# Optimization experiments

Hardware: AMD Instinct MI355X
Metric: run time of the kernel (lower is better)

Reference implementation:

```python
import jax, jax.numpy as jnp
import numpy as np
import math

H = 8
E = 512
D_K = E // H
NEG = -1000000000.0
# last (and only surviving) row of dist_bar: one threshold per head
DIST_BAR = np.array([0.2, 0.3, 0.4, 0.5, 0.6, 0.7, 0.8, 0.9], dtype=np.float32)


def setup_inputs() -> dict:
    key = jax.random.key(0)
    ks = jax.random.split(key, 12)
    B, N = 8, 1024
    s = 1.0 / math.sqrt(E)
    inp = {
        "query": jax.random.normal(ks[0], (B, N, E), jnp.float32),
        "key": jax.random.normal(ks[1], (B, N, E), jnp.float32),
        "value": jax.random.normal(ks[2], (B, N, E), jnp.float32),
        "dist": jax.random.uniform(ks[3], (B, 1, N, N), jnp.float32),
        "mask": jnp.ones((B, N, N), jnp.int32),
        "Wq": jax.random.normal(ks[4], (E, E), jnp.float32) * s,
        "bq": jnp.zeros((E,), jnp.float32),
        "Wk": jax.random.normal(ks[5], (E, E), jnp.float32) * s,
        "bk": jnp.zeros((E,), jnp.float32),
        "Wv": jax.random.normal(ks[6], (E, E), jnp.float32) * s,
        "bv": jnp.zeros((E,), jnp.float32),
        "Wo": jax.random.normal(ks[7], (E, E), jnp.float32) * s,
        "bo": jnp.zeros((E,), jnp.float32),
    }
    return inp


def reference(query, key, value, dist, mask, Wq, bq, Wk, bk, Wv, bv, Wo, bo):
    B, N, _ = query.shape
    # project and split heads: [B, H, N, D_K]
    def heads(x, W, b):
        return (x @ W.T + b).reshape(B, N, H, D_K).transpose(0, 2, 1, 3)
    q = heads(query, Wq, bq)
    k = heads(key, Wk, bk)
    v = heads(value, Wv, bv)
    scores = jnp.einsum("bhqd,bhkd->bhqk", q, k) / math.sqrt(D_K)
    # padding mask: [B,N,N] -> [B,1,N,N]
    scores = jnp.where(mask[:, None, :, :] == 0, NEG, scores)
    # per-head distance mask: dist [B,1,N,N] < thr[h] -> [B,H,N,N]
    thr = jnp.asarray(DIST_BAR)[None, :, None, None]
    dmask = dist < thr
    # first row/col (global atom) always attend
    dmask = dmask.at[:, :, 0, :].set(True).at[:, :, :, 0].set(True)
    scores = jnp.where(dmask, scores, NEG)
    p = jax.nn.softmax(scores, axis=-1)
    out = jnp.einsum("bhqk,bhkd->bhqd", p, v)  # [B,H,N,D_K]
    out = out.transpose(0, 2, 1, 3).reshape(B, N, H * D_K)
    return out @ Wo.T + bo
```

## Files before the change

kernel.cpp:

```cpp
#include <hip/hip_runtime.h>
#include <stdint.h>


typedef __attribute__((ext_vector_type(8))) short short8;
typedef __attribute__((ext_vector_type(4))) float floatx4;

#define MFMA16(a, b, c) __builtin_amdgcn_mfma_f32_16x16x32_bf16((a), (b), (c), 0, 0, 0)
#define QSCALE 0.1803368801111362f

static __device__ __forceinline__ unsigned short f2bf(float f) {
  union { float f; unsigned u; } v; v.f = f;
  unsigned r = v.u + 0x7fffu + ((v.u >> 16) & 1u);
  return (unsigned short)(r >> 16);
}

static __device__ __forceinline__ void gload_lds16(const void* g, void* l) {
  __builtin_amdgcn_global_load_lds((const __attribute__((address_space(1))) unsigned int*)g,
                                   (__attribute__((address_space(3))) unsigned int*)l,
                                   16, 0, 0);
}
static __device__ __forceinline__ int xsw(int row) { return (row & 3) ^ ((row >> 2) & 3); }

__global__ void prep_kernel(const float* __restrict__ q, const float* __restrict__ k,
                            const float* __restrict__ v,
                            const float* __restrict__ wq, const float* __restrict__ wk,
                            const float* __restrict__ wv, const float* __restrict__ wo,
                            const float* __restrict__ dist, const int* __restrict__ mask,
                            unsigned short* __restrict__ qb, unsigned short* __restrict__ kb,
                            unsigned short* __restrict__ vb,
                            unsigned short* __restrict__ wq16, unsigned short* __restrict__ wk16,
                            unsigned short* __restrict__ wv16, unsigned short* __restrict__ wo16,
                            unsigned char* __restrict__ codesP) {
  int gb = blockIdx.x;
  if (gb < 13312) {
    int i = gb * 256 + threadIdx.x;
    const float* s; unsigned short* d; int loc;
    if (i < 3145728) {
      int w = i >> 20; loc = i & 1048575;
      s = (w == 0) ? q : (w == 1) ? k : v;
      d = (w == 0) ? qb : (w == 1) ? kb : vb;
    } else {
      int j = i - 3145728; int w = j >> 16; loc = j & 65535;
      s = (w == 0) ? wq : (w == 1) ? wk : (w == 2) ? wv : wo;
      d = (w == 0) ? wq16 : (w == 1) ? wk16 : (w == 2) ? wv16 : wo16;
    }
    float4 vv = ((const float4*)s)[loc];
    ushort4 o;
    o.x = f2bf(vv.x); o.y = f2bf(vv.y); o.z = f2bf(vv.z); o.w = f2bf(vv.w);
    ((ushort4*)d)[loc] = o;
  } else {
    int t = (gb - 13312) * 256 + threadIdx.x;
    int flat = t << 2;
    int b = flat >> 20;
    int rem = flat & ((1 << 20) - 1);
    int row = rem >> 10;
    int col0 = rem & 1023;
    float4 d4 = ((const float4*)dist)[t];
    int4 m4 = ((const int4*)mask)[t];
    float dv[4] = {d4.x, d4.y, d4.z, d4.w};
    int mv[4] = {m4.x, m4.y, m4.z, m4.w};
    int rg = row >> 5;
    int st = (row >> 4) & 1;
    int qq = (row >> 2) & 3;
    int r = row & 3;
    size_t rowbase = (size_t)(b * 32 + rg) * 32768;
    int sub = st * 32 + r;
#pragma unroll
    for (int u = 0; u < 4; u++) {
      int col = col0 + u;
      float d = dv[u];
      int hmin = (d >= 0.2f) + (d >= 0.3f) + (d >= 0.4f) + (d >= 0.5f) +
                 (d >= 0.6f) + (d >= 0.7f) + (d >= 0.8f) + (d >= 0.9f);
      unsigned char cc = (unsigned char)hmin;
      if (row == 0 || col == 0) cc = 0;
      if (mv[u] == 0) cc = 9;
      int kt = col >> 7, ci = (col >> 4) & 7, c = col & 15;
      int lane = qq * 16 + c;
      codesP[rowbase + (size_t)kt * 4096 + lane * 64 + sub + ci * 4] = cc;
    }
  }
}

__global__ __launch_bounds__(256) void qkv_gemm(
    const unsigned short* __restrict__ Xq, const unsigned short* __restrict__ Xk,
    const unsigned short* __restrict__ Xv,
    const unsigned short* __restrict__ Wqp, const unsigned short* __restrict__ Wkp,
    const unsigned short* __restrict__ Wvp,
    const float* __restrict__ bq, const float* __restrict__ bk, const float* __restrict__ bv,
    unsigned short* __restrict__ Qh, unsigned short* __restrict__ Kh,
    unsigned short* __restrict__ Vt) {
  const int z = blockIdx.z;
  const unsigned short* X = (z == 0) ? Xq : (z == 1) ? Xk : Xv;
  const unsigned short* W = (z == 0) ? Wqp : (z == 1) ? Wkp : Wvp;
  const float* bias = (z == 0) ? bq : (z == 1) ? bk : bv;
  unsigned short* O = (z == 0) ? Qh : (z == 1) ? Kh : Vt;

  __shared__ __align__(16) short Xs[128 * 32];
  __shared__ __align__(16) short Ws[128 * 32];
  const int tid = threadIdx.x;
  const int lane = tid & 63;
  const int wave = tid >> 6;
  const int c = lane & 15;
  const int q = lane >> 4;
  const int m0 = blockIdx.x * 128;
  const int n0 = blockIdx.y * 128;
  const int wr = (wave >> 1) * 64;
  const int wc = (wave & 1) * 64;

  floatx4 acc[4][4];
#pragma unroll
  for (int i = 0; i < 4; i++)
#pragma unroll
    for (int j = 0; j < 4; j++) acc[i][j] = (floatx4)(0.0f);

  for (int k0 = 0; k0 < 512; k0 += 32) {
    __syncthreads();
#pragma unroll
    for (int it = 0; it < 2; it++) {
      int slot = wave * 128 + it * 64 + lane;
      int row = slot >> 2, ch = slot & 3;
      int g = ch ^ xsw(row);
      gload_lds16(X + (size_t)(m0 + row) * 512 + k0 + g * 8, &Xs[(wave * 128 + it * 64) * 8]);
      gload_lds16(W + (size_t)(n0 + row) * 512 + k0 + g * 8, &Ws[(wave * 128 + it * 64) * 8]);
    }
    __syncthreads();

    const short* Pa = (z == 2) ? Xs : Ws;
    const short* Pb = (z == 2) ? Ws : Xs;
    short8 af[4], bfv[4];
#pragma unroll
    for (int i = 0; i < 4; i++) {
      int row = wr + i * 16 + c;
      af[i] = *(const short8*)(&Pa[row * 32 + (q ^ xsw(row)) * 8]);
    }
#pragma unroll
    for (int j = 0; j < 4; j++) {
      int row = wc + j * 16 + c;
      bfv[j] = *(const short8*)(&Pb[row * 32 + (q ^ xsw(row)) * 8]);
    }
#pragma unroll
    for (int i = 0; i < 4; i++)
#pragma unroll
      for (int j = 0; j < 4; j++)
        acc[i][j] = MFMA16(af[i], bfv[j], acc[i][j]);
  }

  if (z == 2) {
#pragma unroll
    for (int i = 0; i < 4; i++) {
      int gm0 = m0 + wr + i * 16 + q * 4;
      int b = gm0 >> 10, n = gm0 & 1023;
#pragma unroll
      for (int j = 0; j < 4; j++) {
        int gn = n0 + wc + j * 16 + c;
        float bb = bias[gn];
        int h = gn >> 6, d = gn & 63;
        ushort4 pk;
#pragma unroll
        for (int r = 0; r < 4; r++) pk[r] = f2bf(acc[i][j][r] + bb);
        *(ushort4*)(&Vt[(((size_t)(b * 8 + h) * 64 + d) << 10) + n]) = pk;
      }
    }
  } else {
    const float scale = (z == 0) ? QSCALE : 1.0f;
#pragma unroll
    for (int i = 0; i < 4; i++) {
      int f0 = n0 + wr + i * 16 + q * 4;
      float4 bb4 = *(const float4*)(bias + f0);
      int h = f0 >> 6, d0 = f0 & 63;
      float bbs[4] = {bb4.x, bb4.y, bb4.z, bb4.w};
#pragma unroll
      for (int j = 0; j < 4; j++) {
        int t = m0 + wc + j * 16 + c;
        int b = t >> 10, n = t & 1023;
        ushort4 pk;
#pragma unroll
        for (int r = 0; r < 4; r++) pk[r] = f2bf((acc[i][j][r] + bbs[r]) * scale);
        *(ushort4*)(&O[((((size_t)(b * 8 + h)) << 10) + n) * 64 + d0]) = pk;
      }
    }
  }
}

__global__ __launch_bounds__(256) void out_gemm(const unsigned short* __restrict__ A,
                                                const unsigned short* __restrict__ W,
                                                const float* __restrict__ bias,
                                                float* __restrict__ Out) {
  __shared__ __align__(16) short As[128 * 32];
  __shared__ __align__(16) short Bs[64 * 32];
  const int tid = threadIdx.x;
  const int lane = tid & 63;
  const int wave = tid >> 6;
  const int c = lane & 15;
  const int q = lane >> 4;
  const int m0 = blockIdx.x * 128;
  const int n0 = blockIdx.y * 64;
  const int wr = (wave >> 1) * 64;
  const int wc = (wave & 1) * 32;

  floatx4 acc[4][2];
#pragma unroll
  for (int i = 0; i < 4; i++)
#pragma unroll
    for (int j = 0; j < 2; j++) acc[i][j] = (floatx4)(0.0f);

  for (int k0 = 0; k0 < 512; k0 += 32) {
    __syncthreads();
#pragma unroll
    for (int it = 0; it < 2; it++) {
      int slot = wave * 128 + it * 64 + lane;
      int row = slot >> 2, ch = slot & 3;
      int g = ch ^ xsw(row);
      gload_lds16(A + (size_t)(m0 + row) * 512 + k0 + g * 8, &As[(wave * 128 + it * 64) * 8]);
    }
    {
      int slot = wave * 64 + lane;
      int row = slot >> 2, ch = slot & 3;
      int g = ch ^ xsw(row);
      gload_lds16(W + (size_t)(n0 + row) * 512 + k0 + g * 8, &Bs[(wave * 64) * 8]);
    }
    __syncthreads();

    short8 af[4], bfv[2];
#pragma unroll
    for (int i = 0; i < 4; i++) {
      int row = wr + i * 16 + c;
      af[i] = *(const short8*)(&As[row * 32 + (q ^ xsw(row)) * 8]);
    }
#pragma unroll
    for (int j = 0; j < 2; j++) {
      int row = wc + j * 16 + c;
      bfv[j] = *(const short8*)(&Bs[row * 32 + (q ^ xsw(row)) * 8]);
    }
#pragma unroll
    for (int i = 0; i < 4; i++)
#pragma unroll
      for (int j = 0; j < 2; j++)
        acc[i][j] = MFMA16(af[i], bfv[j], acc[i][j]);
  }

#pragma unroll
  for (int i = 0; i < 4; i++) {
    int gm0 = m0 + wr + i * 16 + q * 4;
#pragma unroll
    for (int j = 0; j < 2; j++) {
      int gn = n0 + wc + j * 16 + c;
      float bb = bias[gn];
#pragma unroll
      for (int r = 0; r < 4; r++)
        Out[(size_t)(gm0 + r) * 512 + gn] = acc[i][j][r] + bb;
    }
  }
}

__global__ __launch_bounds__(256, 4) void attn_kernel(const unsigned short* __restrict__ Qh,
                                                      const unsigned short* __restrict__ Kh,
                                                      const unsigned short* __restrict__ Vt,
                                                      const unsigned char* __restrict__ codesP,
                                                      unsigned short* __restrict__ AO) {
  __shared__ __align__(16) unsigned short P[4][32 * 132];
  __shared__ float rsx[2][32];
  const int tid = threadIdx.x;
  const int lane = tid & 63;
  const int wave = tid >> 6;
  const int c = lane & 15;
  const int q = lane >> 4;
  const int bh = blockIdx.y;
  const int b = bh >> 3;
  const int h = bh & 7;
  const size_t base = (size_t)bh << 16;
  const int qc = wave >> 1;
  const int kvh = wave & 1;
  const int rbase = blockIdx.x * 64 + qc * 32;
  const int rg = rbase >> 5;
  unsigned short* Pw = &P[wave][0];

  short8 aq[2][2];
#pragma unroll
  for (int st = 0; st < 2; st++)
#pragma unroll
    for (int kk = 0; kk < 2; kk++)
      aq[st][kk] = *(const short8*)(Qh + base + (size_t)(rbase + st * 16 + c) * 64 + kk * 32 + q * 8);

  const unsigned char* cbt = codesP + (size_t)(b * 32 + rg) * 32768 + lane * 64;
  const unsigned short* Kb = Kh + base;
  const unsigned short* Vb = Vt + base;

  float rs[2][4];
#pragma unroll
  for (int st = 0; st < 2; st++)
#pragma unroll
    for (int r = 0; r < 4; r++) rs[st][r] = 0.0f;
  floatx4 o[2][4];
#pragma unroll
  for (int st = 0; st < 2; st++)
#pragma unroll
    for (int ci = 0; ci < 4; ci++) o[st][ci] = (floatx4)(0.0f);

  for (int kt = kvh * 4; kt < kvh * 4 + 4; kt++) {
    const unsigned short* Kt = Kb + (size_t)kt * 128 * 64;
    floatx4 s[2][8];
#pragma unroll
    for (int ci = 0; ci < 8; ci++) { s[0][ci] = (floatx4)(0.0f); s[1][ci] = (floatx4)(0.0f); }
#pragma unroll
    for (int ci = 0; ci < 8; ci++)
#pragma unroll
      for (int kk = 0; kk < 2; kk++) {
        short8 bk = *(const short8*)(Kt + (size_t)(ci * 16 + c) * 64 + kk * 32 + q * 8);
        s[0][ci] = MFMA16(aq[0][kk], bk, s[0][ci]);
        s[1][ci] = MFMA16(aq[1][kk], bk, s[1][ci]);
      }
    const unsigned char* cp = cbt + (size_t)kt * 4096;
    uint4 w0 = *(const uint4*)(cp);
    uint4 w1 = *(const uint4*)(cp + 16);
    uint4 w2 = *(const uint4*)(cp + 32);
    uint4 w3 = *(const uint4*)(cp + 48);
    unsigned cv[16] = {w0.x, w0.y, w0.z, w0.w, w1.x, w1.y, w1.z, w1.w,
                       w2.x, w2.y, w2.z, w2.w, w3.x, w3.y, w3.z, w3.w};
#pragma unroll
    for (int st = 0; st < 2; st++)
#pragma unroll
      for (int ci = 0; ci < 8; ci++)
#pragma unroll
        for (int r = 0; r < 4; r++) {
          int bidx = st * 32 + ci * 4 + r;
          int code = (cv[bidx >> 2] >> ((bidx & 3) * 8)) & 0xff;
          float e = (h >= code) ? exp2f(s[st][ci][r]) : 0.0f;
          rs[st][r] += e;
          Pw[(st * 16 + q * 4 + r) * 132 + ci * 16 + c] = f2bf(e);
        }
#pragma unroll
    for (int ch = 0; ch < 4; ch++) {
      short8 ap0 = *(const short8*)(&Pw[(size_t)c * 132 + ch * 32 + q * 8]);
      short8 ap1 = *(const short8*)(&Pw[(size_t)(16 + c) * 132 + ch * 32 + q * 8]);
#pragma unroll
      for (int ci = 0; ci < 4; ci++) {
        short8 bv = *(const short8*)(Vb + (size_t)(ci * 16 + c) * 1024 + kt * 128 + ch * 32 + q * 8);
        o[0][ci] = MFMA16(ap0, bv, o[0][ci]);
        o[1][ci] = MFMA16(ap1, bv, o[1][ci]);
      }
    }
  }

#pragma unroll
  for (int st = 0; st < 2; st++)
#pragma unroll
    for (int r = 0; r < 4; r++) {
      float v = rs[st][r];
      v += __shfl_xor(v, 1); v += __shfl_xor(v, 2);
      v += __shfl_xor(v, 4); v += __shfl_xor(v, 8);
      rs[st][r] = v;
    }

  float* dump = (float*)&P[qc * 2 + 1][0];
  if (kvh == 1) {
#pragma unroll
    for (int st = 0; st < 2; st++)
#pragma unroll
      for (int ci = 0; ci < 4; ci++)
        *(floatx4*)(dump + lane * 32 + (st * 4 + ci) * 4) = o[st][ci];
    if (c == 0) {
#pragma unroll
      for (int st = 0; st < 2; st++)
#pragma unroll
        for (int r = 0; r < 4; r++) rsx[qc][st * 16 + q * 4 + r] = rs[st][r];
    }
  }
  __syncthreads();
  if (kvh == 0) {
    float inv[2][4];
#pragma unroll
    for (int st = 0; st < 2; st++)
#pragma unroll
      for (int ci = 0; ci < 4; ci++)
        o[st][ci] += *(const floatx4*)(dump + lane * 32 + (st * 4 + ci) * 4);
#pragma unroll
    for (int st = 0; st < 2; st++)
#pragma unroll
      for (int r = 0; r < 4; r++)
        inv[st][r] = 1.0f / (rs[st][r] + rsx[qc][st * 16 + q * 4 + r]);
#pragma unroll
    for (int st = 0; st < 2; st++)
#pragma unroll
      for (int r = 0; r < 4; r++) {
        int n = rbase + st * 16 + q * 4 + r;
        size_t ob = ((size_t)((b << 10) + n)) * 512 + h * 64;
#pragma unroll
        for (int ci = 0; ci < 4; ci++)
          AO[ob + ci * 16 + c] = f2bf(o[st][ci][r] * inv[st][r]);
      }
  }
}

extern "C" void kernel_launch(void* const* d_in, const int* in_sizes, int n_in,
                              void* d_out, int out_size, void* d_ws, size_t ws_size,
                              hipStream_t stream) {
  const float* query = (const float*)d_in[0];
  const float* key_  = (const float*)d_in[1];
  const float* value = (const float*)d_in[2];
  const float* dist  = (const float*)d_in[3];
  const int*   mask  = (const int*)d_in[4];
  const float* Wq = (const float*)d_in[5];
  const float* bq = (const float*)d_in[6];
  const float* Wk = (const float*)d_in[7];
  const float* bk = (const float*)d_in[8];
  const float* Wv = (const float*)d_in[9];
  const float* bv = (const float*)d_in[10];
  const float* Wo = (const float*)d_in[11];
  const float* bo = (const float*)d_in[12];

  char* ws = (char*)d_ws;
  size_t off = 0;
  auto alloc = [&](size_t bytes) -> char* {
    char* p = ws + off;
    off += (bytes + 255) & ~(size_t)255;
    return p;
  };
  const size_t NQKV = 8192ull * 512;
  unsigned short* qb   = (unsigned short*)alloc(NQKV * 2);
  unsigned short* kb   = (unsigned short*)alloc(NQKV * 2);
  unsigned short* vb   = (unsigned short*)alloc(NQKV * 2);
  unsigned short* wq16 = (unsigned short*)alloc(512ull * 512 * 2);
  unsigned short* wk16 = (unsigned short*)alloc(512ull * 512 * 2);
  unsigned short* wv16 = (unsigned short*)alloc(512ull * 512 * 2);
  unsigned short* wo16 = (unsigned short*)alloc(512ull * 512 * 2);
  unsigned short* Qh = (unsigned short*)alloc(NQKV * 2);
  unsigned short* Kh = (unsigned short*)alloc(NQKV * 2);
  unsigned short* Vt = (unsigned short*)alloc(NQKV * 2);
  unsigned short* AO = (unsigned short*)alloc(NQKV * 2);
  unsigned char*  codesP = (unsigned char*)alloc(8ull * 1024 * 1024);

  prep_kernel<<<21504, 256, 0, stream>>>(query, key_, value, Wq, Wk, Wv, Wo, dist, mask,
                                         qb, kb, vb, wq16, wk16, wv16, wo16, codesP);
  qkv_gemm<<<dim3(64, 4, 3), 256, 0, stream>>>(qb, kb, vb, wq16, wk16, wv16,
                                               bq, bk, bv, Qh, Kh, Vt);
  attn_kernel<<<dim3(16, 64), 256, 0, stream>>>(Qh, Kh, Vt, codesP, AO);
  out_gemm<<<dim3(64, 8), 256, 0, stream>>>(AO, wo16, bo, (float*)d_out);
}
```

Baseline: 296.5 us.

## Encode attention mask as per-head bitmasks and split score tiles in halves

The prep kernel now writes the combined padding and distance mask as one 64-bit bitmask per lane and head, instead of one byte code per element. The attention kernel then loads a single u64 per key tile rather than 64 bytes of codes. The score computation is split into two half-tiles to lower register pressure, the launch_bounds occupancy hint is dropped, and the LDS reduction dump is padded to stride 33 to avoid bank conflicts. The new prep mapping has each thread read scattered dist and mask elements with strided, less coalesced accesses. The bitmask buffer is the same size as before.

```diff
diff --git a/kernel.cpp b/kernel.cpp
--- a/kernel.cpp
+++ b/kernel.cpp
@@ -4,6 +4,7 @@
 
 typedef __attribute__((ext_vector_type(8))) short short8;
 typedef __attribute__((ext_vector_type(4))) float floatx4;
+typedef unsigned long long u64;
 
 #define MFMA16(a, b, c) __builtin_amdgcn_mfma_f32_16x16x32_bf16((a), (b), (c), 0, 0, 0)
 #define QSCALE 0.1803368801111362f
@@ -30,7 +31,7 @@
                             unsigned short* __restrict__ vb,
                             unsigned short* __restrict__ wq16, unsigned short* __restrict__ wk16,
                             unsigned short* __restrict__ wv16, unsigned short* __restrict__ wo16,
-                            unsigned char* __restrict__ codesP) {
+                            u64* __restrict__ bits) {
   int gb = blockIdx.x;
   if (gb < 13312) {
     int i = gb * 256 + threadIdx.x;
@@ -49,35 +50,43 @@
     o.x = f2bf(vv.x); o.y = f2bf(vv.y); o.z = f2bf(vv.z); o.w = f2bf(vv.w);
     ((ushort4*)d)[loc] = o;
   } else {
-    int t = (gb - 13312) * 256 + threadIdx.x;
-    int flat = t << 2;
-    int b = flat >> 20;
-    int rem = flat & ((1 << 20) - 1);
-    int row = rem >> 10;
-    int col0 = rem & 1023;
-    float4 d4 = ((const float4*)dist)[t];
-    int4 m4 = ((const int4*)mask)[t];
-    float dv[4] = {d4.x, d4.y, d4.z, d4.w};
-    int mv[4] = {m4.x, m4.y, m4.z, m4.w};
-    int rg = row >> 5;
-    int st = (row >> 4) & 1;
-    int qq = (row >> 2) & 3;
-    int r = row & 3;
-    size_t rowbase = (size_t)(b * 32 + rg) * 32768;
-    int sub = st * 32 + r;
-#pragma unroll
-    for (int u = 0; u < 4; u++) {
-      int col = col0 + u;
-      float d = dv[u];
-      int hmin = (d >= 0.2f) + (d >= 0.3f) + (d >= 0.4f) + (d >= 0.5f) +
-                 (d >= 0.6f) + (d >= 0.7f) + (d >= 0.8f) + (d >= 0.9f);
-      unsigned char cc = (unsigned char)hmin;
-      if (row == 0 || col == 0) cc = 0;
-      if (mv[u] == 0) cc = 9;
-      int kt = col >> 7, ci = (col >> 4) & 7, c = col & 15;
-      int lane = qq * 16 + c;
-      codesP[rowbase + (size_t)kt * 4096 + lane * 64 + sub + ci * 4] = cc;
-    }
+    int bx = gb - 13312;
+    int ktp = bx & 1;
+    int brg = bx >> 1;
+    int bb = brg >> 5, rg = brg & 31;
+    int kt = ktp * 4 + (threadIdx.x >> 6);
+    int lane = threadIdx.x & 63;
+    int qq = lane >> 4, cc = lane & 15;
+    const float* db = dist + ((size_t)bb << 20);
+    const int* mb = mask + ((size_t)bb << 20);
+    unsigned lo[8] = {0, 0, 0, 0, 0, 0, 0, 0};
+    unsigned hi[8] = {0, 0, 0, 0, 0, 0, 0, 0};
+#pragma unroll
+    for (int st = 0; st < 2; st++)
+#pragma unroll
+      for (int ci = 0; ci < 8; ci++) {
+        int col = kt * 128 + ci * 16 + cc;
+#pragma unroll
+        for (int r = 0; r < 4; r++) {
+          int row = rg * 32 + st * 16 + qq * 4 + r;
+          float d = db[((size_t)row << 10) + col];
+          int m = mb[((size_t)row << 10) + col];
+          int code = (d >= 0.2f) + (d >= 0.3f) + (d >= 0.4f) + (d >= 0.5f) +
+                     (d >= 0.6f) + (d >= 0.7f) + (d >= 0.8f) + (d >= 0.9f);
+          if (row == 0 || col == 0) code = 0;
+          if (m == 0) code = 9;
+          unsigned ab = (0xFFu << code) & 0xFFu;
+          int pos = ci * 4 + r;
+#pragma unroll
+          for (int h = 0; h < 8; h++) {
+            unsigned bit = ((ab >> h) & 1u) << pos;
+            if (st == 0) lo[h] |= bit; else hi[h] |= bit;
+          }
+        }
+      }
+    u64* wout = bits + (((size_t)brg * 8 + kt) * 64 + lane) * 8;
+#pragma unroll
+    for (int h = 0; h < 8; h++) wout[h] = (u64)lo[h] | ((u64)hi[h] << 32);
   }
 }
 
@@ -253,11 +262,11 @@
   }
 }
 
-__global__ __launch_bounds__(256, 4) void attn_kernel(const unsigned short* __restrict__ Qh,
-                                                      const unsigned short* __restrict__ Kh,
-                                                      const unsigned short* __restrict__ Vt,
-                                                      const unsigned char* __restrict__ codesP,
-                                                      unsigned short* __restrict__ AO) {
+__global__ __launch_bounds__(256) void attn_kernel(const unsigned short* __restrict__ Qh,
+                                                   const unsigned short* __restrict__ Kh,
+                                                   const unsigned short* __restrict__ Vt,
+                                                   const u64* __restrict__ bits,
+                                                   unsigned short* __restrict__ AO) {
   __shared__ __align__(16) unsigned short P[4][32 * 132];
   __shared__ float rsx[2][32];
   const int tid = threadIdx.x;
@@ -282,7 +291,7 @@
     for (int kk = 0; kk < 2; kk++)
       aq[st][kk] = *(const short8*)(Qh + base + (size_t)(rbase + st * 16 + c) * 64 + kk * 32 + q * 8);
 
-  const unsigned char* cbt = codesP + (size_t)(b * 32 + rg) * 32768 + lane * 64;
+  const u64* wb = bits + (((size_t)(b * 32 + rg) * 8) * 64 + lane) * 8 + h;
   const unsigned short* Kb = Kh + base;
   const unsigned short* Vb = Vt + base;
 
@@ -299,36 +308,38 @@
 
   for (int kt = kvh * 4; kt < kvh * 4 + 4; kt++) {
     const unsigned short* Kt = Kb + (size_t)kt * 128 * 64;
-    floatx4 s[2][8];
-#pragma unroll
-    for (int ci = 0; ci < 8; ci++) { s[0][ci] = (floatx4)(0.0f); s[1][ci] = (floatx4)(0.0f); }
-#pragma unroll
-    for (int ci = 0; ci < 8; ci++)
-#pragma unroll
-      for (int kk = 0; kk < 2; kk++) {
-        short8 bk = *(const short8*)(Kt + (size_t)(ci * 16 + c) * 64 + kk * 32 + q * 8);
-        s[0][ci] = MFMA16(aq[0][kk], bk, s[0][ci]);
-        s[1][ci] = MFMA16(aq[1][kk], bk, s[1][ci]);
-      }
-    const unsigned char* cp = cbt + (size_t)kt * 4096;
-    uint4 w0 = *(const uint4*)(cp);
-    uint4 w1 = *(const uint4*)(cp + 16);
-    uint4 w2 = *(const uint4*)(cp + 32);
-    uint4 w3 = *(const uint4*)(cp + 48);
-    unsigned cv[16] = {w0.x, w0.y, w0.z, w0.w, w1.x, w1.y, w1.z, w1.w,
-                       w2.x, w2.y, w2.z, w2.w, w3.x, w3.y, w3.z, w3.w};
-#pragma unroll
-    for (int st = 0; st < 2; st++)
-#pragma unroll
-      for (int ci = 0; ci < 8; ci++)
-#pragma unroll
-        for (int r = 0; r < 4; r++) {
-          int bidx = st * 32 + ci * 4 + r;
-          int code = (cv[bidx >> 2] >> ((bidx & 3) * 8)) & 0xff;
-          float e = (h >= code) ? exp2f(s[st][ci][r]) : 0.0f;
-          rs[st][r] += e;
-          Pw[(st * 16 + q * 4 + r) * 132 + ci * 16 + c] = f2bf(e);
+    u64 w64 = wb[(size_t)kt * 512];
+    unsigned wlo = (unsigned)w64, whi = (unsigned)(w64 >> 32);
+#pragma unroll
+    for (int hf = 0; hf < 2; hf++) {
+      floatx4 s[2][4];
+#pragma unroll
+      for (int c2 = 0; c2 < 4; c2++) { s[0][c2] = (floatx4)(0.0f); s[1][c2] = (floatx4)(0.0f); }
+#pragma unroll
+      for (int c2 = 0; c2 < 4; c2++) {
+        int ci = hf * 4 + c2;
+#pragma unroll
+        for (int kk = 0; kk < 2; kk++) {
+          short8 bk = *(const short8*)(Kt + (size_t)(ci * 16 + c) * 64 + kk * 32 + q * 8);
+          s[0][c2] = MFMA16(aq[0][kk], bk, s[0][c2]);
+          s[1][c2] = MFMA16(aq[1][kk], bk, s[1][c2]);
         }
+      }
+#pragma unroll
+      for (int st = 0; st < 2; st++) {
+        unsigned sel = st ? whi : wlo;
+#pragma unroll
+        for (int c2 = 0; c2 < 4; c2++) {
+          int ci = hf * 4 + c2;
+#pragma unroll
+          for (int r = 0; r < 4; r++) {
+            float e = ((sel >> (ci * 4 + r)) & 1u) ? exp2f(s[st][c2][r]) : 0.0f;
+            rs[st][r] += e;
+            Pw[(st * 16 + q * 4 + r) * 132 + ci * 16 + c] = f2bf(e);
+          }
+        }
+      }
+    }
 #pragma unroll
     for (int ch = 0; ch < 4; ch++) {
       short8 ap0 = *(const short8*)(&Pw[(size_t)c * 132 + ch * 32 + q * 8]);
@@ -358,7 +369,9 @@
     for (int st = 0; st < 2; st++)
 #pragma unroll
       for (int ci = 0; ci < 4; ci++)
-        *(floatx4*)(dump + lane * 32 + (st * 4 + ci) * 4) = o[st][ci];
+#pragma unroll
+        for (int r = 0; r < 4; r++)
+          dump[lane * 33 + (st * 4 + ci) * 4 + r] = o[st][ci][r];
     if (c == 0) {
 #pragma unroll
       for (int st = 0; st < 2; st++)
@@ -373,7 +386,9 @@
     for (int st = 0; st < 2; st++)
 #pragma unroll
       for (int ci = 0; ci < 4; ci++)
-        o[st][ci] += *(const floatx4*)(dump + lane * 32 + (st * 4 + ci) * 4);
+#pragma unroll
+        for (int r = 0; r < 4; r++)
+          o[st][ci][r] += dump[lane * 33 + (st * 4 + ci) * 4 + r];
 #pragma unroll
     for (int st = 0; st < 2; st++)
 #pragma unroll
@@ -428,12 +443,12 @@
   unsigned short* Kh = (unsigned short*)alloc(NQKV * 2);
   unsigned short* Vt = (unsigned short*)alloc(NQKV * 2);
   unsigned short* AO = (unsigned short*)alloc(NQKV * 2);
-  unsigned char*  codesP = (unsigned char*)alloc(8ull * 1024 * 1024);
-
-  prep_kernel<<<21504, 256, 0, stream>>>(query, key_, value, Wq, Wk, Wv, Wo, dist, mask,
-                                         qb, kb, vb, wq16, wk16, wv16, wo16, codesP);
+  u64*            bits = (u64*)alloc(8ull * 1024 * 1024);
+
+  prep_kernel<<<13824, 256, 0, stream>>>(query, key_, value, Wq, Wk, Wv, Wo, dist, mask,
+                                         qb, kb, vb, wq16, wk16, wv16, wo16, bits);
   qkv_gemm<<<dim3(64, 4, 3), 256, 0, stream>>>(qb, kb, vb, wq16, wk16, wv16,
                                                bq, bk, bv, Qh, Kh, Vt);
-  attn_kernel<<<dim3(16, 64), 256, 0, stream>>>(Qh, Kh, Vt, codesP, AO);
+  attn_kernel<<<dim3(16, 64), 256, 0, stream>>>(Qh, Kh, Vt, bits, AO);
   out_gemm<<<dim3(64, 8), 256, 0, stream>>>(AO, wo16, bo, (float*)d_out);
 }
```

Result: slower. 332.9 us (+12.3%).
